# Kernel tuning notes

Hardware: AMD Instinct MI355X
Metric: run time of the kernel (lower is better)

Reference implementation:

```python
import jax, jax.numpy as jnp
import numpy as np

# ---- model constants (match init_kwargs) ----
NX, NY, H, K, GRID = 32, 1, 64, 3, 5
MID = 2 * H + 1            # 129, middle width of each KAN block
NB = GRID + K              # 8 B-spline basis functions per edge
BATCH = 65536


def _grid_pts():
    # uniform extended grid on [-1, 1] with K extra knots each side: GRID+2K+1 pts
    step = 2.0 / GRID
    return jnp.arange(-K, GRID + K + 1, dtype=jnp.float32) * step - 1.0


def bspline_basis(x):
    """Cox-de Boor B-spline bases. x: [B, I] -> [B, I, GRID+K]."""
    g = _grid_pts()[None, None, :]          # [1,1,P]
    xe = x[..., None]                       # [B,I,1]
    B0 = ((xe >= g[..., :-1]) & (xe < g[..., 1:])).astype(x.dtype)
    Bp = B0
    for p in range(1, K + 1):
        left = (xe - g[..., :-(p + 1)]) / (g[..., p:-1] - g[..., :-(p + 1)])
        right = (g[..., p + 1:] - xe) / (g[..., p + 1:] - g[..., 1:-p])
        Bp = left * Bp[..., :-1] + right * Bp[..., 1:]
    return Bp  # [B, I, NB]


def kan_layer(x, coef, sb, ss, bias):
    """pykan KANLayer: y_o = sum_i sb[i,o]*silu(x_i) + ss[i,o]*spline_io(x_i) + bias_o.
    x: [B,I]; coef: [I,O,NB]; sb, ss: [I,O]; bias: [O]."""
    bs = bspline_basis(x)                                   # [B,I,NB]
    spline = jnp.einsum('bip,iop->bo', bs, coef * ss[:, :, None])
    return jax.nn.silu(x) @ sb + spline + bias


def setup_inputs() -> dict:
    key = jax.random.key(0)
    ks = iter(jax.random.split(key, 40))

    def xavier(k, shape, fan_in, fan_out):
        gain = np.sqrt(2.0)  # relu gain, as in the torch module
        std = gain * np.sqrt(2.0 / (fan_in + fan_out))
        return (std * jax.random.normal(k, shape, dtype=jnp.float32))

    inp = {
        'x': jax.random.normal(next(ks), (BATCH, NX), dtype=jnp.float32),
        'W_in': xavier(next(ks), (NX, H), NX, H),
        'b_in': jnp.zeros((H,), jnp.float32),
        'W_out': xavier(next(ks), (H, NY), H, NY),
    }
    for l in range(2):  # num_hidden_layers KAN blocks, each = 2 KANLayers
        for tag, (din, dout) in [('a', (H, MID)), ('b', (MID, H))]:
            inp[f'coef{l}{tag}'] = xavier(next(ks), (din, dout, NB), din * NB, dout)
            inp[f'sb{l}{tag}'] = xavier(next(ks), (din, dout), din, dout)
            inp[f'ss{l}{tag}'] = jnp.ones((din, dout), jnp.float32)
            inp[f'bias{l}{tag}'] = jnp.zeros((dout,), jnp.float32)
    return inp


def reference(x, W_in, b_in, W_out,
              coef0a, sb0a, ss0a, bias0a, coef0b, sb0b, ss0b, bias0b,
              coef1a, sb1a, ss1a, bias1a, coef1b, sb1b, ss1b, bias1b):
    h = jax.nn.relu(x @ W_in + b_in)
    for (ca, sa, ta, ba, cb, sbb, tb, bb) in (
        (coef0a, sb0a, ss0a, bias0a, coef0b, sb0b, ss0b, bias0b),
        (coef1a, sb1a, ss1a, bias1a, coef1b, sb1b, ss1b, bias1b),
    ):
        h = kan_layer(h, ca, sa, ta, ba)   # H -> 2H+1
        h = kan_layer(h, cb, sbb, tb, bb)  # 2H+1 -> H
    return jax.nn.sigmoid(h @ W_out)       # [B, NY]
```

## Files before the change

### kernel.cpp

```cpp
#include <hip/hip_runtime.h>
#include <math.h>
#include <stdint.h>

#define BATCH 65536
#define TB 64

typedef _Float16 half8 __attribute__((ext_vector_type(8)));
typedef float   floatx4 __attribute__((ext_vector_type(4)));

#define SH 68
#define SM 130
#define HM_SLICE (16*SM + 64)

#define WIN 2048
#define KSA 18
#define KSB 39
#define WA (KSA*9*512)
#define WB (KSB*4*512)
#define WTOT (WIN + 2*(WA+WB))

__global__ void setup_weights(
    const float* __restrict__ W_in,
    const float* __restrict__ c0a, const float* __restrict__ sb0a, const float* __restrict__ ss0a,
    const float* __restrict__ c0b, const float* __restrict__ sb0b, const float* __restrict__ ss0b,
    const float* __restrict__ c1a, const float* __restrict__ sb1a, const float* __restrict__ ss1a,
    const float* __restrict__ c1b, const float* __restrict__ sb1b, const float* __restrict__ ss1b,
    _Float16* __restrict__ wt) {
  int idx = blockIdx.x * 256 + threadIdx.x;
  if (idx >= WTOT) return;
  float v = 0.0f;
  if (idx < WIN) {
    int nt = idx >> 9; int r = idx & 511; int l = r >> 3; int j = r & 7;
    int n = nt*16 + (l & 15);
    int k = (l >> 4)*8 + j;
    v = W_in[k*64 + n];
  } else {
    int e2   = idx - WIN;
    int pair = (e2 >= WA + WB) ? 1 : 0;
    int e    = e2 - pair * (WA + WB);
    if (e < WA) {
      const float* coef = pair ? c1a : c0a;
      const float* sb   = pair ? sb1a : sb0a;
      const float* ss   = pair ? ss1a : ss0a;
      int ks = e / 4608; int r = e - ks*4608;
      int nt = r >> 9;   int q = r & 511;
      int l  = q >> 3;   int j = q & 7;
      int n  = nt*16 + (l & 15);
      int k  = ks*32 + (l >> 4)*8 + j;
      if (n < 129) {
        if (k < 512) { int i = k >> 3, p = k & 7; v = ss[i*129+n] * coef[(i*129+n)*8 + p]; }
        else         { int i = k - 512;           v = sb[i*129+n]; }
      }
    } else {
      const float* coef = pair ? c1b : c0b;
      const float* sb   = pair ? sb1b : sb0b;
      const float* ss   = pair ? ss1b : ss0b;
      int eb = e - WA;
      int ks = eb >> 11; int r = eb & 2047;
      int nt = r >> 9;   int q = r & 511;
      int l  = q >> 3;   int j = q & 7;
      int n  = nt*16 + (l & 15);
      int k  = ks*32 + (l >> 4)*8 + j;
      if (k < 1088) { int i = k >> 3, p = k & 7; if (i < 129) v = ss[i*64+n] * coef[(i*64+n)*8 + p]; }
      else          { int i = k - 1088;          if (i < 129) v = sb[i*64+n]; }
    }
  }
  wt[idx] = (_Float16)v;
}

__device__ __forceinline__ half8 feat8(float x) {
  float s  = (x + 2.2f) * 2.5f;
  float mf = floorf(s);
  int   m  = (int)mf;
  float u  = s - mf;
  float t  = 1.0f - u;
  float u2 = u*u;
  float w0 = t*t*t * (1.0f/6.0f);
  float w3 = u2*u * (1.0f/6.0f);
  float w1 = fmaf(u2, fmaf(0.5f, u, -1.0f), 2.0f/3.0f);
  float w2 = 1.0f - w0 - w1 - w3;
  union { _Float16 h[4]; uint64_t u; } P;
  P.h[0] = (_Float16)w0; P.h[1] = (_Float16)w1;
  P.h[2] = (_Float16)w2; P.h[3] = (_Float16)w3;
  uint64_t w01 = (m >= 0 && m <= 10) ? P.u : 0ull;
  int sh = (m - 3) * 16;
  uint64_t q0 = (sh >= 0) ? ((sh < 64) ? (w01 << sh) : 0ull) : (w01 >> (-sh));
  uint64_t q1 = (sh >= 64) ? (w01 << (sh - 64))
                           : ((sh > 0) ? (w01 >> (64 - sh)) : 0ull);
  union { uint64_t q[2]; half8 h; } R;
  R.q[0] = q0; R.q[1] = q1;
  return R.h;
}

template<int KSPL, int KSIL, int NT, int SIN, int O, int SOUT>
__device__ __forceinline__ void kan_layer(
    const _Float16* __restrict__ hinw, _Float16* __restrict__ houtw,
    const _Float16* __restrict__ wt, const float* __restrict__ bias, int lane) {
  const int ln = lane & 15;
  const int kq = lane >> 4;
  floatx4 acc[NT];
  #pragma unroll
  for (int j = 0; j < NT; ++j) acc[j] = (floatx4){0.f, 0.f, 0.f, 0.f};

  #pragma unroll 2
  for (int ks = 0; ks < KSPL; ++ks) {
    float xv = (float)hinw[ln*SIN + ks*4 + kq];
    half8 A = feat8(xv);
    #pragma unroll
    for (int j = 0; j < NT; ++j) {
      half8 B = *(const half8*)&wt[((ks*NT + j) << 9) + lane*8];
      acc[j] = __builtin_amdgcn_mfma_f32_16x16x32_f16(A, B, acc[j], 0, 0, 0);
    }
  }

  #pragma unroll 2
  for (int sk = 0; sk < KSIL; ++sk) {
    half8 h8 = *(const half8*)&hinw[ln*SIN + sk*32 + kq*8];
    half8 A;
    #pragma unroll
    for (int e = 0; e < 8; ++e) {
      float xv = (float)h8[e];
      A[e] = (_Float16)(xv / (1.0f + __expf(-xv)));
    }
    #pragma unroll
    for (int j = 0; j < NT; ++j) {
      half8 B = *(const half8*)&wt[(((KSPL + sk)*NT + j) << 9) + lane*8];
      acc[j] = __builtin_amdgcn_mfma_f32_16x16x32_f16(A, B, acc[j], 0, 0, 0);
    }
  }

  #pragma unroll
  for (int j = 0; j < NT; ++j) {
    int col = j*16 + ln;
    if (col < O) {
      float bv = bias[col];
      #pragma unroll
      for (int r = 0; r < 4; ++r)
        houtw[(kq*4 + r)*SOUT + col] = (_Float16)(acc[j][r] + bv);
    }
  }
}

extern "C" __global__ void __launch_bounds__(256, 4)
kan_forward(const float* __restrict__ x, const float* __restrict__ b_in,
            const float* __restrict__ W_out, const _Float16* __restrict__ wt,
            const float* __restrict__ bias0a, const float* __restrict__ bias0b,
            const float* __restrict__ bias1a, const float* __restrict__ bias1b,
            float* __restrict__ out) {
  __shared__ _Float16 hM[4][HM_SLICE];
  __shared__ _Float16 hH[4][16*SH];
  const int t    = threadIdx.x;
  const int wv   = t >> 6;
  const int lane = t & 63;
  const int ln   = lane & 15;
  const int kq   = lane >> 4;
  _Float16* hMw = hM[wv];
  _Float16* hHw = hH[wv];
  const int rbase = blockIdx.x * TB + wv * 16;

  hMw[16*SM + lane] = (_Float16)0.0f;
  if (lane < 16) hMw[lane*SM + 129] = (_Float16)0.0f;

  {
    const float* xr = &x[(rbase + ln)*32 + kq*8];
    float4 v0 = *(const float4*)&xr[0];
    float4 v1 = *(const float4*)&xr[4];
    half8 A = { (_Float16)v0.x, (_Float16)v0.y, (_Float16)v0.z, (_Float16)v0.w,
                (_Float16)v1.x, (_Float16)v1.y, (_Float16)v1.z, (_Float16)v1.w };
    #pragma unroll
    for (int nt = 0; nt < 4; ++nt) {
      floatx4 z = (floatx4){0.f, 0.f, 0.f, 0.f};
      half8 B = *(const half8*)&wt[(nt << 9) + lane*8];
      floatx4 a = __builtin_amdgcn_mfma_f32_16x16x32_f16(A, B, z, 0, 0, 0);
      int col = nt*16 + ln;
      float bv = b_in[col];
      #pragma unroll
      for (int r = 0; r < 4; ++r)
        hHw[(kq*4 + r)*SH + col] = (_Float16)fmaxf(a[r] + bv, 0.0f);
    }
  }

  kan_layer<16,2,9,SH,129,SM>(hHw, hMw, wt + WIN,             bias0a, lane);
  kan_layer<34,5,4,SM, 64,SH>(hMw, hHw, wt + WIN + WA,        bias0b, lane);
  kan_layer<16,2,9,SH,129,SM>(hHw, hMw, wt + WIN + WA + WB,   bias1a, lane);
  kan_layer<34,5,4,SM, 64,SH>(hMw, hHw, wt + WIN + 2*WA + WB, bias1b, lane);

  {
    float s = 0.0f;
    #pragma unroll
    for (int j = 0; j < 16; ++j)
      s = fmaf((float)hHw[ln*SH + kq*16 + j], W_out[kq*16 + j], s);
    s += __shfl_down(s, 32);
    s += __shfl_down(s, 16);
    if (lane < 16) out[rbase + ln] = 1.0f / (1.0f + __expf(-s));
  }
}

extern "C" void kernel_launch(void* const* d_in, const int* in_sizes, int n_in,
                              void* d_out, int out_size, void* d_ws, size_t ws_size,
                              hipStream_t stream) {
  const float* x     = (const float*)d_in[0];
  const float* W_in  = (const float*)d_in[1];
  const float* b_in  = (const float*)d_in[2];
  const float* W_out = (const float*)d_in[3];
  const float* c0a = (const float*)d_in[4];  const float* sb0a = (const float*)d_in[5];
  const float* ss0a= (const float*)d_in[6];  const float* bias0a=(const float*)d_in[7];
  const float* c0b = (const float*)d_in[8];  const float* sb0b = (const float*)d_in[9];
  const float* ss0b= (const float*)d_in[10]; const float* bias0b=(const float*)d_in[11];
  const float* c1a = (const float*)d_in[12]; const float* sb1a = (const float*)d_in[13];
  const float* ss1a= (const float*)d_in[14]; const float* bias1a=(const float*)d_in[15];
  const float* c1b = (const float*)d_in[16]; const float* sb1b = (const float*)d_in[17];
  const float* ss1b= (const float*)d_in[18]; const float* bias1b=(const float*)d_in[19];
  float*    out = (float*)d_out;
  _Float16* wt  = (_Float16*)d_ws;

  setup_weights<<<(WTOT + 255)/256, 256, 0, stream>>>(
      W_in, c0a, sb0a, ss0a, c0b, sb0b, ss0b,
      c1a, sb1a, ss1a, c1b, sb1b, ss1b, wt);

  kan_forward<<<BATCH/TB, 256, 0, stream>>>(
      x, b_in, W_out, wt, bias0a, bias0b, bias1a, bias1b, out);
}
```

Measured before the change: 188.3 us.

## Process two 16-row tiles per wave to reuse weight fragments across MFMAs

Each wave now handles 32 batch rows instead of 16, keeping two accumulator sets so each loaded B weight fragment feeds two MFMAs. This halves global/L2 weight traffic per row and the block count. The four KAN layer calls are folded into a non-unrolled loop, which shrinks code size. The costs are double the accumulator registers and LDS per wave, with launch bounds lowered to 2 blocks per SM, so occupancy drops.

```diff
diff --git a/kernel.cpp b/kernel.cpp
--- a/kernel.cpp
+++ b/kernel.cpp
@@ -3,14 +3,14 @@
 #include <stdint.h>
 
 #define BATCH 65536
-#define TB 64
+#define TB 128
 
 typedef _Float16 half8 __attribute__((ext_vector_type(8)));
 typedef float   floatx4 __attribute__((ext_vector_type(4)));
 
 #define SH 68
 #define SM 130
-#define HM_SLICE (16*SM + 64)
+#define HM_SLICE (32*SM + 64)
 
 #define WIN 2048
 #define KSA 18
@@ -98,34 +98,43 @@
     const _Float16* __restrict__ wt, const float* __restrict__ bias, int lane) {
   const int ln = lane & 15;
   const int kq = lane >> 4;
-  floatx4 acc[NT];
+  floatx4 acc0[NT], acc1[NT];
   #pragma unroll
-  for (int j = 0; j < NT; ++j) acc[j] = (floatx4){0.f, 0.f, 0.f, 0.f};
+  for (int j = 0; j < NT; ++j) {
+    acc0[j] = (floatx4){0.f, 0.f, 0.f, 0.f};
+    acc1[j] = (floatx4){0.f, 0.f, 0.f, 0.f};
+  }
 
   #pragma unroll 2
   for (int ks = 0; ks < KSPL; ++ks) {
-    float xv = (float)hinw[ln*SIN + ks*4 + kq];
-    half8 A = feat8(xv);
+    float xv0 = (float)hinw[ ln      *SIN + ks*4 + kq];
+    float xv1 = (float)hinw[(16 + ln)*SIN + ks*4 + kq];
+    half8 A0 = feat8(xv0);
+    half8 A1 = feat8(xv1);
     #pragma unroll
     for (int j = 0; j < NT; ++j) {
       half8 B = *(const half8*)&wt[((ks*NT + j) << 9) + lane*8];
-      acc[j] = __builtin_amdgcn_mfma_f32_16x16x32_f16(A, B, acc[j], 0, 0, 0);
+      acc0[j] = __builtin_amdgcn_mfma_f32_16x16x32_f16(A0, B, acc0[j], 0, 0, 0);
+      acc1[j] = __builtin_amdgcn_mfma_f32_16x16x32_f16(A1, B, acc1[j], 0, 0, 0);
     }
   }
 
   #pragma unroll 2
   for (int sk = 0; sk < KSIL; ++sk) {
-    half8 h8 = *(const half8*)&hinw[ln*SIN + sk*32 + kq*8];
-    half8 A;
+    half8 h0 = *(const half8*)&hinw[ ln      *SIN + sk*32 + kq*8];
+    half8 h1 = *(const half8*)&hinw[(16 + ln)*SIN + sk*32 + kq*8];
+    half8 A0, A1;
     #pragma unroll
     for (int e = 0; e < 8; ++e) {
-      float xv = (float)h8[e];
-      A[e] = (_Float16)(xv / (1.0f + __expf(-xv)));
+      float x0 = (float)h0[e], x1 = (float)h1[e];
+      A0[e] = (_Float16)(x0 / (1.0f + __expf(-x0)));
+      A1[e] = (_Float16)(x1 / (1.0f + __expf(-x1)));
     }
     #pragma unroll
     for (int j = 0; j < NT; ++j) {
       half8 B = *(const half8*)&wt[(((KSPL + sk)*NT + j) << 9) + lane*8];
-      acc[j] = __builtin_amdgcn_mfma_f32_16x16x32_f16(A, B, acc[j], 0, 0, 0);
+      acc0[j] = __builtin_amdgcn_mfma_f32_16x16x32_f16(A0, B, acc0[j], 0, 0, 0);
+      acc1[j] = __builtin_amdgcn_mfma_f32_16x16x32_f16(A1, B, acc1[j], 0, 0, 0);
     }
   }
 
@@ -135,20 +144,22 @@
     if (col < O) {
       float bv = bias[col];
       #pragma unroll
-      for (int r = 0; r < 4; ++r)
-        houtw[(kq*4 + r)*SOUT + col] = (_Float16)(acc[j][r] + bv);
-    }
-  }
-}
-
-extern "C" __global__ void __launch_bounds__(256, 4)
+      for (int r = 0; r < 4; ++r) {
+        houtw[(      kq*4 + r)*SOUT + col] = (_Float16)(acc0[j][r] + bv);
+        houtw[(16 + kq*4 + r)*SOUT + col] = (_Float16)(acc1[j][r] + bv);
+      }
+    }
+  }
+}
+
+extern "C" __global__ void __launch_bounds__(256, 2)
 kan_forward(const float* __restrict__ x, const float* __restrict__ b_in,
             const float* __restrict__ W_out, const _Float16* __restrict__ wt,
             const float* __restrict__ bias0a, const float* __restrict__ bias0b,
             const float* __restrict__ bias1a, const float* __restrict__ bias1b,
             float* __restrict__ out) {
   __shared__ _Float16 hM[4][HM_SLICE];
-  __shared__ _Float16 hH[4][16*SH];
+  __shared__ _Float16 hH[4][32*SH];
   const int t    = threadIdx.x;
   const int wv   = t >> 6;
   const int lane = t & 63;
@@ -156,43 +167,57 @@
   const int kq   = lane >> 4;
   _Float16* hMw = hM[wv];
   _Float16* hHw = hH[wv];
-  const int rbase = blockIdx.x * TB + wv * 16;
-
-  hMw[16*SM + lane] = (_Float16)0.0f;
-  if (lane < 16) hMw[lane*SM + 129] = (_Float16)0.0f;
+  const int rbase = blockIdx.x * TB + wv * 32;
+
+  hMw[32*SM + lane] = (_Float16)0.0f;
+  if (lane < 32) hMw[lane*SM + 129] = (_Float16)0.0f;
 
   {
-    const float* xr = &x[(rbase + ln)*32 + kq*8];
-    float4 v0 = *(const float4*)&xr[0];
-    float4 v1 = *(const float4*)&xr[4];
-    half8 A = { (_Float16)v0.x, (_Float16)v0.y, (_Float16)v0.z, (_Float16)v0.w,
-                (_Float16)v1.x, (_Float16)v1.y, (_Float16)v1.z, (_Float16)v1.w };
+    const float* xr0 = &x[(rbase + ln     )*32 + kq*8];
+    const float* xr1 = &x[(rbase + 16 + ln)*32 + kq*8];
+    float4 a0 = *(const float4*)&xr0[0];
+    float4 a1 = *(const float4*)&xr0[4];
+    float4 b0 = *(const float4*)&xr1[0];
+    float4 b1 = *(const float4*)&xr1[4];
+    half8 A0 = { (_Float16)a0.x, (_Float16)a0.y, (_Float16)a0.z, (_Float16)a0.w,
+                 (_Float16)a1.x, (_Float16)a1.y, (_Float16)a1.z, (_Float16)a1.w };
+    half8 A1 = { (_Float16)b0.x, (_Float16)b0.y, (_Float16)b0.z, (_Float16)b0.w,
+                 (_Float16)b1.x, (_Float16)b1.y, (_Float16)b1.z, (_Float16)b1.w };
     #pragma unroll
     for (int nt = 0; nt < 4; ++nt) {
       floatx4 z = (floatx4){0.f, 0.f, 0.f, 0.f};
       half8 B = *(const half8*)&wt[(nt << 9) + lane*8];
-      floatx4 a = __builtin_amdgcn_mfma_f32_16x16x32_f16(A, B, z, 0, 0, 0);
+      floatx4 c0 = __builtin_amdgcn_mfma_f32_16x16x32_f16(A0, B, z, 0, 0, 0);
+      floatx4 c1 = __builtin_amdgcn_mfma_f32_16x16x32_f16(A1, B, z, 0, 0, 0);
       int col = nt*16 + ln;
       float bv = b_in[col];
       #pragma unroll
-      for (int r = 0; r < 4; ++r)
-        hHw[(kq*4 + r)*SH + col] = (_Float16)fmaxf(a[r] + bv, 0.0f);
-    }
-  }
-
-  kan_layer<16,2,9,SH,129,SM>(hHw, hMw, wt + WIN,             bias0a, lane);
-  kan_layer<34,5,4,SM, 64,SH>(hMw, hHw, wt + WIN + WA,        bias0b, lane);
-  kan_layer<16,2,9,SH,129,SM>(hHw, hMw, wt + WIN + WA + WB,   bias1a, lane);
-  kan_layer<34,5,4,SM, 64,SH>(hMw, hHw, wt + WIN + 2*WA + WB, bias1b, lane);
+      for (int r = 0; r < 4; ++r) {
+        hHw[(      kq*4 + r)*SH + col] = (_Float16)fmaxf(c0[r] + bv, 0.0f);
+        hHw[(16 + kq*4 + r)*SH + col] = (_Float16)fmaxf(c1[r] + bv, 0.0f);
+      }
+    }
+  }
+
+  const _Float16* wp = wt + WIN;
+  #pragma unroll 1
+  for (int rep = 0; rep < 2; ++rep) {
+    const float* ba = rep ? bias1a : bias0a;
+    const float* bb = rep ? bias1b : bias0b;
+    kan_layer<16,2,9,SH,129,SM>(hHw, hMw, wp,      ba, lane);
+    kan_layer<34,5,4,SM, 64,SH>(hMw, hHw, wp + WA, bb, lane);
+    wp += WA + WB;
+  }
 
   {
+    int row = lane & 31;
+    int kh  = lane >> 5;
     float s = 0.0f;
     #pragma unroll
-    for (int j = 0; j < 16; ++j)
-      s = fmaf((float)hHw[ln*SH + kq*16 + j], W_out[kq*16 + j], s);
+    for (int j = 0; j < 32; ++j)
+      s = fmaf((float)hHw[row*SH + kh*32 + j], W_out[kh*32 + j], s);
     s += __shfl_down(s, 32);
-    s += __shfl_down(s, 16);
-    if (lane < 16) out[rbase + ln] = 1.0f / (1.0f + __expf(-s));
+    if (lane < 32) out[rbase + row] = 1.0f / (1.0f + __expf(-s));
   }
 }
 
```

After: 211.3 us. +12.2%, slower.
